# Optimization experiments

Measured on AMD Instinct MI355X. Metric: run time of the kernel, lower is better.

The kernel has to match this reference:

```python
import jax, jax.numpy as jnp
import numpy as np

LMAX = 2
C1 = 64; C2 = 64; COUT = 64
B = 4096
SUM_RDIM = sum(3**L for L in range(LMAX + 1))   # 13
FEAT1 = C1 * SUM_RDIM                            # 832
FEAT2 = C2 * SUM_RDIM


def _enumerate_paths(Lmax):
    paths = []
    for L1 in range(Lmax + 1):
        for L2 in range(Lmax + 1):
            for k in range(min(L1, L2) + 1):
                Lout = L1 + L2 - 2 * k
                if 0 <= Lout <= Lmax:
                    paths.append((L1, L2, Lout, k, False))
            if L1 >= 1 and L2 >= 1:
                for k in range(min(L1 - 1, L2 - 1) + 1):
                    Lout = L1 + L2 - 2 * k - 1
                    if 0 <= Lout <= Lmax:
                        paths.append((L1, L2, Lout, k, True))
    return paths

PATHS = _enumerate_paths(LMAX)   # 15 paths for Lmax=2


def _path_eq(L1, L2, k, use_eps):
    # Fused equation: W[c,a,b] contracted together with the delta/eps path einsum.
    letters = list('defghijklmnopqrstuvwxyz')  # a,b,c reserved for channels
    i_idx = letters[:L1]
    j_idx = letters[L1:L1 + L2]
    for r in range(k):  # delta: contract last k indices of A with last k of B
        j_idx[L2 - k + r] = i_idx[L1 - k + r]
    i_free = i_idx[:L1 - k]
    j_free = j_idx[:L2 - k]
    eps_sub = None
    if use_eps:  # consume last free index of each side via eps_{p i j}
        p = letters[L1 + L2]
        eps_sub = p + i_free[-1] + j_free[-1]
        i_free, j_free = i_free[:-1], j_free[:-1]
        out = i_free + j_free + [p]
    else:
        out = i_free + j_free
    terms = ['cab', '...a' + ''.join(i_idx), '...b' + ''.join(j_idx)]
    if eps_sub is not None:
        terms.append(eps_sub)
    return ','.join(terms) + '->...c' + ''.join(out)


def _epsilon():
    e = np.zeros((3, 3, 3), dtype=np.float32)
    e[0, 1, 2] = e[1, 2, 0] = e[2, 0, 1] = 1.0
    e[2, 1, 0] = e[1, 0, 2] = e[0, 2, 1] = -1.0
    return jnp.asarray(e)


def _split_by_rank(x, C, Lmax):
    batch = x.shape[:-1]
    out, idx = {}, 0
    for L in range(Lmax + 1):
        d = C * 3**L
        blk = x[..., idx:idx + d]
        idx += d
        out[L] = blk.reshape(*batch, C) if L == 0 else blk.reshape(*batch, C, *((3,) * L))
    return out


def setup_inputs() -> dict:
    key = jax.random.key(0)
    k1, k2, k3 = jax.random.split(key, 3)
    x1 = jax.random.normal(k1, (B, FEAT1), dtype=jnp.float32)
    x2 = jax.random.normal(k2, (B, FEAT2), dtype=jnp.float32)
    weight = jax.random.normal(k3, (len(PATHS) * COUT * C1 * C2,), dtype=jnp.float32) * 0.02
    return {"x1": x1, "x2": x2, "weight": weight}


def reference(x1, x2, weight):
    A = _split_by_rank(x1, C1, LMAX)
    Bt = _split_by_rank(x2, C2, LMAX)
    eps = _epsilon().astype(x1.dtype)
    batch = x1.shape[:-1]
    blocks = {L: jnp.zeros((*batch, COUT) + (3,) * L, dtype=x1.dtype) for L in range(LMAX + 1)}
    wsz = COUT * C1 * C2
    for n, (L1, L2, Lout, k, use_eps) in enumerate(PATHS):
        Wp = weight[n * wsz:(n + 1) * wsz].reshape(COUT, C1, C2)
        eq = _path_eq(L1, L2, k, use_eps)
        ops = (Wp, A[L1], Bt[L2]) + ((eps,) if use_eps else ())
        blocks[Lout] = blocks[Lout] + jnp.einsum(eq, *ops, optimize='optimal')
    parts = [blocks[L].reshape(*batch, COUT * 3**L) for L in range(LMAX + 1)]
    return jnp.concatenate(parts, axis=-1)
```

## Files before the change

### kernel.cpp

```cpp
#include <hip/hip_runtime.h>
#include <cstdint>
#include <cstddef>


#define FEAT 832
#define ZT 64

typedef _Float16 half8 __attribute__((ext_vector_type(8)));
typedef float floatx16 __attribute__((ext_vector_type(16)));

struct Chunk {
  int wbase;
  int o1[3];
  int o2[3];
  float sg[3];
  int d1, d2, nt;
};

__global__ void swz_w_kernel(const float* __restrict__ w, _Float16* __restrict__ o) {
  const int i = blockIdx.x * 256 + threadIdx.x;
  const int lane = i & 63;
  const int pkc  = i >> 6;
  const int cgrp = pkc & 1;
  const int ksg  = (pkc >> 1) & 255;
  const int p    = pkc >> 9;
  const int c  = cgrp * 32 + (lane & 31);
  const int k0 = ksg * 16 + (lane >> 5) * 8;
  const float* src = w + (size_t)p * 262144 + (size_t)c * 4096 + k0;
  const float4 v0 = *(const float4*)(src);
  const float4 v1 = *(const float4*)(src + 4);
  half8 h = { (_Float16)v0.x, (_Float16)v0.y, (_Float16)v0.z, (_Float16)v0.w,
              (_Float16)v1.x, (_Float16)v1.y, (_Float16)v1.z, (_Float16)v1.w };
  *(half8*)(o + (size_t)i * 8) = h;
}

__global__ __launch_bounds__(256) void gather_kernel(
    float* __restrict__ out, const float* __restrict__ part, int np)
{
  __shared__ float T[64][65];
  const int zb = blockIdx.x * 64;
  const int fb = blockIdx.y * 64;
  const int tid = threadIdx.x;
  const int fl = tid >> 6;
  const int zl = tid & 63;
  #pragma unroll
  for (int i = 0; i < 16; ++i) {
    const int f = fb + fl + i * 4;
    int s, c;
    if (f < 64)       { s = 0;              c = f; }
    else if (f < 256) { const int g = f - 64;  c = g / 3; s = 1 + g % 3; }
    else              { const int g = f - 256; c = g / 9; s = 4 + g % 9; }
    const size_t base = (size_t)s * 262144 + (size_t)c * 4096 + zb + zl;
    float v = 0.0f;
    for (int q = 0; q < np; ++q)
      v += part[(size_t)q * 3407872 + base];
    T[fl + i * 4][zl] = v;
  }
  __syncthreads();
  const int zr = tid >> 6;
  const int fc = tid & 63;
  #pragma unroll
  for (int i = 0; i < 16; ++i) {
    const int z = zr + i * 4;
    float* o = out + (size_t)(zb + z) * FEAT + fb + fc;
    *o += T[fc][z];
  }
}

__device__ __forceinline__ half8 splat8(_Float16 h) {
  return half8{h, h, h, h, h, h, h, h};
}

template<int NT>
__device__ __forceinline__ void run_chunk(
    const Chunk C, const int zbase, const int zl, const int hf,
    const int lane, const int tid, const int a0,
    const float* __restrict__ x1, const float* __restrict__ x2,
    const _Float16* __restrict__ Wh,
    _Float16* __restrict__ XS2, _Float16* __restrict__ XS1,
    floatx16& acc0, floatx16& acc1)
{
  __syncthreads();

  #pragma unroll
  for (int t = 0; t < NT; ++t) {
    const size_t base2 = (size_t)zbase * FEAT + C.o2[t];
    for (int e = tid; e < 4096; e += 256) {
      const int zz = e >> 6, b = e & 63;
      XS2[(t * 64 + zz) * 72 + b] =
          (_Float16)x2[base2 + (size_t)zz * FEAT + b * C.d2];
    }
  }
  #pragma unroll
  for (int t = 0; t < NT; ++t) {
    const float sgf = C.sg[t];
    const int o1 = C.o1[t];
    for (int e = tid; e < 4096; e += 256) {
      const int a = e & 63, zz = e >> 6;
      XS1[(t * 64 + a) * 66 + zz] =
          (_Float16)(x1[(size_t)(zbase + zz) * FEAT + o1 + a * C.d1] * sgf);
    }
  }
  __syncthreads();

  half8 x2r[NT][4];
  #pragma unroll
  for (int t = 0; t < NT; ++t) {
    #pragma unroll
    for (int ks = 0; ks < 4; ++ks)
      x2r[t][ks] = *(const half8*)&XS2[(t * 64 + zl) * 72 + ks * 16 + hf * 8];
  }

  const _Float16* __restrict__ Wq = Wh + C.wbase + lane * 8;
  const _Float16* __restrict__ Xq = XS1 + zl;

  half8 afE[2][4], afO[2][4];
  const _Float16* __restrict__ w0 = Wq + (size_t)a0 * 4096;
  #pragma unroll
  for (int ks = 0; ks < 4; ++ks) {
    afE[0][ks] = *(const half8*)(w0 + ks * 1024);
    afE[1][ks] = *(const half8*)(w0 + ks * 1024 + 512);
    afO[0][ks] = *(const half8*)(w0 + 4096 + ks * 1024);
    afO[1][ks] = *(const half8*)(w0 + 4096 + ks * 1024 + 512);
  }
  _Float16 sc[NT], scn[NT];
  #pragma unroll
  for (int t = 0; t < NT; ++t) {
    sc[t]  = Xq[(t * 64 + a0) * 66];
    scn[t] = Xq[(t * 64 + a0 + 1) * 66];
  }

  const int aend = a0 + 32;
  #pragma unroll 1
  for (int a = a0; a < aend; a += 2) {
    {
      half8 sv[NT];
      #pragma unroll
      for (int t = 0; t < NT; ++t) sv[t] = splat8(sc[t]);
      if (a + 2 < aend) {
        #pragma unroll
        for (int t = 0; t < NT; ++t) sc[t] = Xq[(t * 64 + a + 2) * 66];
      }
      #pragma unroll
      for (int ks = 0; ks < 4; ++ks) {
        half8 tb = sv[0] * x2r[0][ks];
        if (NT > 1) tb += sv[1] * x2r[1][ks];
        if (NT > 2) tb += sv[2] * x2r[2][ks];
        acc0 = __builtin_amdgcn_mfma_f32_32x32x16_f16(afE[0][ks], tb, acc0, 0, 0, 0);
        acc1 = __builtin_amdgcn_mfma_f32_32x32x16_f16(afE[1][ks], tb, acc1, 0, 0, 0);
      }
      if (a + 2 < aend) {
        const _Float16* wn = Wq + (size_t)(a + 2) * 4096;
        #pragma unroll
        for (int ks = 0; ks < 4; ++ks) {
          afE[0][ks] = *(const half8*)(wn + ks * 1024);
          afE[1][ks] = *(const half8*)(wn + ks * 1024 + 512);
        }
      }
    }
    {
      half8 sv[NT];
      #pragma unroll
      for (int t = 0; t < NT; ++t) sv[t] = splat8(scn[t]);
      if (a + 3 < aend) {
        #pragma unroll
        for (int t = 0; t < NT; ++t) scn[t] = Xq[(t * 64 + a + 3) * 66];
      }
      #pragma unroll
      for (int ks = 0; ks < 4; ++ks) {
        half8 tb = sv[0] * x2r[0][ks];
        if (NT > 1) tb += sv[1] * x2r[1][ks];
        if (NT > 2) tb += sv[2] * x2r[2][ks];
        acc0 = __builtin_amdgcn_mfma_f32_32x32x16_f16(afO[0][ks], tb, acc0, 0, 0, 0);
        acc1 = __builtin_amdgcn_mfma_f32_32x32x16_f16(afO[1][ks], tb, acc1, 0, 0, 0);
      }
      if (a + 3 < aend) {
        const _Float16* wn = Wq + (size_t)(a + 3) * 4096;
        #pragma unroll
        for (int ks = 0; ks < 4; ++ks) {
          afO[0][ks] = *(const half8*)(wn + ks * 1024);
          afO[1][ks] = *(const half8*)(wn + ks * 1024 + 512);
        }
      }
    }
  }
}

__global__ __launch_bounds__(256, 2) void tp_kernel(
    const float* __restrict__ x1, const float* __restrict__ x2,
    const _Float16* __restrict__ Wh, float* __restrict__ out,
    float* __restrict__ part)
{
  __shared__ __align__(16) _Float16 XS2[3 * 64 * 72];
  __shared__ __align__(16) _Float16 XS1[3 * 64 * 66];
  __shared__ Chunk chs[7];
  __shared__ int nch_s;

  const int tid  = threadIdx.x;
  const int slot = blockIdx.y;
  const int q    = blockIdx.z;
  const int nsplit = gridDim.z;
  const int zbase = blockIdx.x * ZT;
  const int wid  = tid >> 6;
  const int zgrp = wid & 1;
  const int ah   = wid >> 1;
  const int a0   = ah * 32;
  const int lane = tid & 63;
  const int ln31 = lane & 31;
  const int hf   = lane >> 5;
  const int zl   = zgrp * 32 + ln31;

  int offO, dO, mO;
  if (slot == 0)      { offO = 0;   dO = 1; mO = 0; }
  else if (slot < 4)  { offO = 64;  dO = 3; mO = slot - 1; }
  else                { offO = 256; dO = 9; mO = slot - 4; }

  if (tid == 0) {
    int n = 0;
    auto add = [&](int p, int L1, int L2,
                   int i0, int i1, int i2, int j0, int j1, int j2,
                   float s0, float s1, float s2, int nt) {
      const int offs[3] = {0, 64, 256};
      const int ds[3]   = {1, 3, 9};
      Chunk c;
      c.wbase = p * 262144;
      c.o1[0] = offs[L1] + i0; c.o1[1] = offs[L1] + i1; c.o1[2] = offs[L1] + i2;
      c.o2[0] = offs[L2] + j0; c.o2[1] = offs[L2] + j1; c.o2[2] = offs[L2] + j2;
      c.sg[0] = s0; c.sg[1] = s1; c.sg[2] = s2;
      c.d1 = ds[L1]; c.d2 = ds[L2]; c.nt = nt;
      chs[n++] = c;
    };
    if (slot == 0) {
      add(0, 0,0, 0,0,0, 0,0,0, 1,0,0, 1);
      add(5, 1,1, 0,1,2, 0,1,2, 1,1,1, 3);
      add(13,2,2, 0,1,2, 0,1,2, 1,1,1, 3);
      add(13,2,2, 3,4,5, 3,4,5, 1,1,1, 3);
      add(13,2,2, 6,7,8, 6,7,8, 1,1,1, 3);
    } else if (slot < 4) {
      const int m = slot - 1, p1 = (m+1)%3, p2 = (m+2)%3;
      add(1, 0,1, 0,0,0, m,0,0, 1,0,0, 1);
      add(3, 1,0, m,0,0, 0,0,0, 1,0,0, 1);
      add(6, 1,1, p1,p2,0, p2,p1,0, 1,-1,0, 2);
      add(7, 1,2, 0,1,2, 3*m,3*m+1,3*m+2, 1,1,1, 3);
      add(10,2,1, 3*m,3*m+1,3*m+2, 0,1,2, 1,1,1, 3);
      add(14,2,2, 3*p1,3*p1+1,3*p1+2, 3*p2,3*p2+1,3*p2+2, 1,1,1, 3);
      add(14,2,2, 3*p2,3*p2+1,3*p2+2, 3*p1,3*p1+1,3*p1+2, -1,-1,-1, 3);
    } else {
      const int m = slot - 4, u = m/3, v = m%3, q1 = (v+1)%3, q2 = (v+2)%3;
      add(2, 0,2, 0,0,0, m,0,0, 1,0,0, 1);
      add(4, 1,1, u,0,0, v,0,0, 1,0,0, 1);
      add(8, 1,2, q1,q2,0, 3*u+q2,3*u+q1,0, 1,-1,0, 2);
      add(9, 2,0, m,0,0, 0,0,0, 1,0,0, 1);
      add(11,2,1, 3*u+q1,3*u+q2,0, q2,q1,0, 1,-1,0, 2);
      add(12,2,2, 3*u,3*u+1,3*u+2, 3*v,3*v+1,3*v+2, 1,1,1, 3);
    }
    nch_s = n;
  }
  __syncthreads();
  const int nch = nch_s;

  floatx16 acc0, acc1;
  #pragma unroll
  for (int r = 0; r < 16; ++r) { acc0[r] = 0.0f; acc1[r] = 0.0f; }

  for (int ci = q; ci < nch; ci += nsplit) {
    const Chunk C = chs[ci];
    if (C.nt == 1)      run_chunk<1>(C, zbase, zl, hf, lane, tid, a0, x1, x2, Wh, XS2, XS1, acc0, acc1);
    else if (C.nt == 2) run_chunk<2>(C, zbase, zl, hf, lane, tid, a0, x1, x2, Wh, XS2, XS1, acc0, acc1);
    else                run_chunk<3>(C, zbase, zl, hf, lane, tid, a0, x1, x2, Wh, XS2, XS1, acc0, acc1);
  }

  __syncthreads();
  float* R = (float*)XS2;
  if (ah == 1) {
    #pragma unroll
    for (int r = 0; r < 16; ++r) {
      R[r * 128 + zgrp * 64 + lane]        = acc0[r];
      R[(16 + r) * 128 + zgrp * 64 + lane] = acc1[r];
    }
  }
  __syncthreads();
  if (ah == 0) {
    #pragma unroll
    for (int r = 0; r < 16; ++r) {
      acc0[r] += R[r * 128 + zgrp * 64 + lane];
      acc1[r] += R[(16 + r) * 128 + zgrp * 64 + lane];
    }

    if (q == 0) {
      float* __restrict__ op = out + (size_t)(zbase + zl) * FEAT + offO + mO;
      #pragma unroll
      for (int r = 0; r < 16; ++r) {
        const int cr = (r & 3) + 8 * (r >> 2) + 4 * hf;
        op[(size_t)cr * dO]        = acc0[r];
        op[(size_t)(cr + 32) * dO] = acc1[r];
      }
    } else {
      float* __restrict__ op = part + (size_t)(q - 1) * 3407872
                                    + (size_t)slot * 262144 + (zbase + zl);
      #pragma unroll
      for (int r = 0; r < 16; ++r) {
        const int cr = (r & 3) + 8 * (r >> 2) + 4 * hf;
        op[(size_t)cr * 4096]        = acc0[r];
        op[(size_t)(cr + 32) * 4096] = acc1[r];
      }
    }
  }
}

extern "C" void kernel_launch(void* const* d_in, const int* in_sizes, int n_in,
                              void* d_out, int out_size, void* d_ws, size_t ws_size,
                              hipStream_t stream) {
  const float* x1 = (const float*)d_in[0];
  const float* x2 = (const float*)d_in[1];
  const float* w  = (const float*)d_in[2];
  float* out = (float*)d_out;
  _Float16* Wh = (_Float16*)d_ws;
  float* part = (float*)((char*)d_ws + 7864320);

  const size_t plane_bytes = 3407872ull * 4ull;
  int np = (ws_size > 7864320) ? (int)((ws_size - 7864320) / plane_bytes) : 1;
  if (np > 3) np = 3;
  if (np < 1) np = 1;
  const int nsplit = np + 1;

  const int nchunks = 15 * 64 * 4096 / 8;
  hipLaunchKernelGGL(swz_w_kernel, dim3(nchunks / 256), dim3(256), 0, stream, w, Wh);

  dim3 grid(64, 13, nsplit);
  hipLaunchKernelGGL(tp_kernel, grid, dim3(256), 0, stream, x1, x2, Wh, out, part);

  dim3 ggrid(64, 13);
  hipLaunchKernelGGL(gather_kernel, ggrid, dim3(256), 0, stream, out, part, np);
}
```

Measured before the change: 420.0 us.

## Merge z-groups into one wave to reuse weight fragments across both z halves

Shrinks the tp_kernel block from four waves to two. Each wave now covers both 32-row z halves with four accumulators instead of two, so every weight fragment loaded from global memory feeds two MFMAs instead of one, halving per-block weight traffic. The cost is higher register pressure (four 16-float accumulators plus doubled x2 fragments), fewer threads for the shared-memory staging loops, and fewer waves per block for latency hiding.

Result: faster. 411.3 us (-2.1%).

```diff
diff --git a/kernel.cpp b/kernel.cpp
--- a/kernel.cpp
+++ b/kernel.cpp
@@ -73,19 +73,19 @@
 
 template<int NT>
 __device__ __forceinline__ void run_chunk(
-    const Chunk C, const int zbase, const int zl, const int hf,
+    const Chunk C, const int zbase, const int ln31, const int hf,
     const int lane, const int tid, const int a0,
     const float* __restrict__ x1, const float* __restrict__ x2,
     const _Float16* __restrict__ Wh,
     _Float16* __restrict__ XS2, _Float16* __restrict__ XS1,
-    floatx16& acc0, floatx16& acc1)
+    floatx16& acc00, floatx16& acc01, floatx16& acc10, floatx16& acc11)
 {
   __syncthreads();
 
   #pragma unroll
   for (int t = 0; t < NT; ++t) {
     const size_t base2 = (size_t)zbase * FEAT + C.o2[t];
-    for (int e = tid; e < 4096; e += 256) {
+    for (int e = tid; e < 4096; e += 128) {
       const int zz = e >> 6, b = e & 63;
       XS2[(t * 64 + zz) * 72 + b] =
           (_Float16)x2[base2 + (size_t)zz * FEAT + b * C.d2];
@@ -95,7 +95,7 @@
   for (int t = 0; t < NT; ++t) {
     const float sgf = C.sg[t];
     const int o1 = C.o1[t];
-    for (int e = tid; e < 4096; e += 256) {
+    for (int e = tid; e < 4096; e += 128) {
       const int a = e & 63, zz = e >> 6;
       XS1[(t * 64 + a) * 66 + zz] =
           (_Float16)(x1[(size_t)(zbase + zz) * FEAT + o1 + a * C.d1] * sgf);
@@ -103,16 +103,18 @@
   }
   __syncthreads();
 
-  half8 x2r[NT][4];
-  #pragma unroll
-  for (int t = 0; t < NT; ++t) {
+  half8 x2r[NT][2][4];
+  #pragma unroll
+  for (int t = 0; t < NT; ++t)
     #pragma unroll
-    for (int ks = 0; ks < 4; ++ks)
-      x2r[t][ks] = *(const half8*)&XS2[(t * 64 + zl) * 72 + ks * 16 + hf * 8];
-  }
+    for (int zh = 0; zh < 2; ++zh)
+      #pragma unroll
+      for (int ks = 0; ks < 4; ++ks)
+        x2r[t][zh][ks] =
+            *(const half8*)&XS2[(t * 64 + zh * 32 + ln31) * 72 + ks * 16 + hf * 8];
 
   const _Float16* __restrict__ Wq = Wh + C.wbase + lane * 8;
-  const _Float16* __restrict__ Xq = XS1 + zl;
+  const _Float16* __restrict__ Xq = XS1 + ln31;
 
   half8 afE[2][4], afO[2][4];
   const _Float16* __restrict__ w0 = Wq + (size_t)a0 * 4096;
@@ -123,31 +125,42 @@
     afO[0][ks] = *(const half8*)(w0 + 4096 + ks * 1024);
     afO[1][ks] = *(const half8*)(w0 + 4096 + ks * 1024 + 512);
   }
-  _Float16 sc[NT], scn[NT];
-  #pragma unroll
-  for (int t = 0; t < NT; ++t) {
-    sc[t]  = Xq[(t * 64 + a0) * 66];
-    scn[t] = Xq[(t * 64 + a0 + 1) * 66];
-  }
+  _Float16 sc[NT][2], scn[NT][2];
+  #pragma unroll
+  for (int t = 0; t < NT; ++t)
+    #pragma unroll
+    for (int zh = 0; zh < 2; ++zh) {
+      sc[t][zh]  = Xq[(t * 64 + a0) * 66 + zh * 32];
+      scn[t][zh] = Xq[(t * 64 + a0 + 1) * 66 + zh * 32];
+    }
 
   const int aend = a0 + 32;
   #pragma unroll 1
   for (int a = a0; a < aend; a += 2) {
     {
-      half8 sv[NT];
-      #pragma unroll
-      for (int t = 0; t < NT; ++t) sv[t] = splat8(sc[t]);
+      half8 sv[NT][2];
+      #pragma unroll
+      for (int t = 0; t < NT; ++t) {
+        sv[t][0] = splat8(sc[t][0]);
+        sv[t][1] = splat8(sc[t][1]);
+      }
       if (a + 2 < aend) {
         #pragma unroll
-        for (int t = 0; t < NT; ++t) sc[t] = Xq[(t * 64 + a + 2) * 66];
+        for (int t = 0; t < NT; ++t) {
+          sc[t][0] = Xq[(t * 64 + a + 2) * 66];
+          sc[t][1] = Xq[(t * 64 + a + 2) * 66 + 32];
+        }
       }
       #pragma unroll
       for (int ks = 0; ks < 4; ++ks) {
-        half8 tb = sv[0] * x2r[0][ks];
-        if (NT > 1) tb += sv[1] * x2r[1][ks];
-        if (NT > 2) tb += sv[2] * x2r[2][ks];
-        acc0 = __builtin_amdgcn_mfma_f32_32x32x16_f16(afE[0][ks], tb, acc0, 0, 0, 0);
-        acc1 = __builtin_amdgcn_mfma_f32_32x32x16_f16(afE[1][ks], tb, acc1, 0, 0, 0);
+        half8 tb0 = sv[0][0] * x2r[0][0][ks];
+        half8 tb1 = sv[0][1] * x2r[0][1][ks];
+        if (NT > 1) { tb0 += sv[1][0] * x2r[1][0][ks]; tb1 += sv[1][1] * x2r[1][1][ks]; }
+        if (NT > 2) { tb0 += sv[2][0] * x2r[2][0][ks]; tb1 += sv[2][1] * x2r[2][1][ks]; }
+        acc00 = __builtin_amdgcn_mfma_f32_32x32x16_f16(afE[0][ks], tb0, acc00, 0, 0, 0);
+        acc01 = __builtin_amdgcn_mfma_f32_32x32x16_f16(afE[0][ks], tb1, acc01, 0, 0, 0);
+        acc10 = __builtin_amdgcn_mfma_f32_32x32x16_f16(afE[1][ks], tb0, acc10, 0, 0, 0);
+        acc11 = __builtin_amdgcn_mfma_f32_32x32x16_f16(afE[1][ks], tb1, acc11, 0, 0, 0);
       }
       if (a + 2 < aend) {
         const _Float16* wn = Wq + (size_t)(a + 2) * 4096;
@@ -159,20 +172,29 @@
       }
     }
     {
-      half8 sv[NT];
-      #pragma unroll
-      for (int t = 0; t < NT; ++t) sv[t] = splat8(scn[t]);
+      half8 sv[NT][2];
+      #pragma unroll
+      for (int t = 0; t < NT; ++t) {
+        sv[t][0] = splat8(scn[t][0]);
+        sv[t][1] = splat8(scn[t][1]);
+      }
       if (a + 3 < aend) {
         #pragma unroll
-        for (int t = 0; t < NT; ++t) scn[t] = Xq[(t * 64 + a + 3) * 66];
+        for (int t = 0; t < NT; ++t) {
+          scn[t][0] = Xq[(t * 64 + a + 3) * 66];
+          scn[t][1] = Xq[(t * 64 + a + 3) * 66 + 32];
+        }
       }
       #pragma unroll
       for (int ks = 0; ks < 4; ++ks) {
-        half8 tb = sv[0] * x2r[0][ks];
-        if (NT > 1) tb += sv[1] * x2r[1][ks];
-        if (NT > 2) tb += sv[2] * x2r[2][ks];
-        acc0 = __builtin_amdgcn_mfma_f32_32x32x16_f16(afO[0][ks], tb, acc0, 0, 0, 0);
-        acc1 = __builtin_amdgcn_mfma_f32_32x32x16_f16(afO[1][ks], tb, acc1, 0, 0, 0);
+        half8 tb0 = sv[0][0] * x2r[0][0][ks];
+        half8 tb1 = sv[0][1] * x2r[0][1][ks];
+        if (NT > 1) { tb0 += sv[1][0] * x2r[1][0][ks]; tb1 += sv[1][1] * x2r[1][1][ks]; }
+        if (NT > 2) { tb0 += sv[2][0] * x2r[2][0][ks]; tb1 += sv[2][1] * x2r[2][1][ks]; }
+        acc00 = __builtin_amdgcn_mfma_f32_32x32x16_f16(afO[0][ks], tb0, acc00, 0, 0, 0);
+        acc01 = __builtin_amdgcn_mfma_f32_32x32x16_f16(afO[0][ks], tb1, acc01, 0, 0, 0);
+        acc10 = __builtin_amdgcn_mfma_f32_32x32x16_f16(afO[1][ks], tb0, acc10, 0, 0, 0);
+        acc11 = __builtin_amdgcn_mfma_f32_32x32x16_f16(afO[1][ks], tb1, acc11, 0, 0, 0);
       }
       if (a + 3 < aend) {
         const _Float16* wn = Wq + (size_t)(a + 3) * 4096;
@@ -186,7 +208,7 @@
   }
 }
 
-__global__ __launch_bounds__(256, 2) void tp_kernel(
+__global__ __launch_bounds__(128, 2) void tp_kernel(
     const float* __restrict__ x1, const float* __restrict__ x2,
     const _Float16* __restrict__ Wh, float* __restrict__ out,
     float* __restrict__ part)
@@ -201,14 +223,11 @@
   const int q    = blockIdx.z;
   const int nsplit = gridDim.z;
   const int zbase = blockIdx.x * ZT;
-  const int wid  = tid >> 6;
-  const int zgrp = wid & 1;
-  const int ah   = wid >> 1;
+  const int ah   = tid >> 6;
   const int a0   = ah * 32;
   const int lane = tid & 63;
   const int ln31 = lane & 31;
   const int hf   = lane >> 5;
-  const int zl   = zgrp * 32 + ln31;
 
   int offO, dO, mO;
   if (slot == 0)      { offO = 0;   dO = 1; mO = 0; }
@@ -259,15 +278,23 @@
   __syncthreads();
   const int nch = nch_s;
 
-  floatx16 acc0, acc1;
-  #pragma unroll
-  for (int r = 0; r < 16; ++r) { acc0[r] = 0.0f; acc1[r] = 0.0f; }
+  floatx16 acc00, acc01, acc10, acc11;
+  #pragma unroll
+  for (int r = 0; r < 16; ++r) {
+    acc00[r] = 0.0f; acc01[r] = 0.0f; acc10[r] = 0.0f; acc11[r] = 0.0f;
+  }
 
   for (int ci = q; ci < nch; ci += nsplit) {
     const Chunk C = chs[ci];
-    if (C.nt == 1)      run_chunk<1>(C, zbase, zl, hf, lane, tid, a0, x1, x2, Wh, XS2, XS1, acc0, acc1);
-    else if (C.nt == 2) run_chunk<2>(C, zbase, zl, hf, lane, tid, a0, x1, x2, Wh, XS2, XS1, acc0, acc1);
-    else                run_chunk<3>(C, zbase, zl, hf, lane, tid, a0, x1, x2, Wh, XS2, XS1, acc0, acc1);
+    if (C.nt == 1)
+      run_chunk<1>(C, zbase, ln31, hf, lane, tid, a0, x1, x2, Wh, XS2, XS1,
+                   acc00, acc01, acc10, acc11);
+    else if (C.nt == 2)
+      run_chunk<2>(C, zbase, ln31, hf, lane, tid, a0, x1, x2, Wh, XS2, XS1,
+                   acc00, acc01, acc10, acc11);
+    else
+      run_chunk<3>(C, zbase, ln31, hf, lane, tid, a0, x1, x2, Wh, XS2, XS1,
+                   acc00, acc01, acc10, acc11);
   }
 
   __syncthreads();
@@ -275,34 +302,44 @@
   if (ah == 1) {
     #pragma unroll
     for (int r = 0; r < 16; ++r) {
-      R[r * 128 + zgrp * 64 + lane]        = acc0[r];
-      R[(16 + r) * 128 + zgrp * 64 + lane] = acc1[r];
+      R[(0 * 16 + r) * 64 + lane] = acc00[r];
+      R[(1 * 16 + r) * 64 + lane] = acc01[r];
+      R[(2 * 16 + r) * 64 + lane] = acc10[r];
+      R[(3 * 16 + r) * 64 + lane] = acc11[r];
     }
   }
   __syncthreads();
   if (ah == 0) {
     #pragma unroll
     for (int r = 0; r < 16; ++r) {
-      acc0[r] += R[r * 128 + zgrp * 64 + lane];
-      acc1[r] += R[(16 + r) * 128 + zgrp * 64 + lane];
+      acc00[r] += R[(0 * 16 + r) * 64 + lane];
+      acc01[r] += R[(1 * 16 + r) * 64 + lane];
+      acc10[r] += R[(2 * 16 + r) * 64 + lane];
+      acc11[r] += R[(3 * 16 + r) * 64 + lane];
     }
 
     if (q == 0) {
-      float* __restrict__ op = out + (size_t)(zbase + zl) * FEAT + offO + mO;
+      float* __restrict__ op0 = out + (size_t)(zbase + ln31) * FEAT + offO + mO;
+      float* __restrict__ op1 = out + (size_t)(zbase + 32 + ln31) * FEAT + offO + mO;
       #pragma unroll
       for (int r = 0; r < 16; ++r) {
         const int cr = (r & 3) + 8 * (r >> 2) + 4 * hf;
-        op[(size_t)cr * dO]        = acc0[r];
-        op[(size_t)(cr + 32) * dO] = acc1[r];
+        op0[(size_t)cr * dO]        = acc00[r];
+        op0[(size_t)(cr + 32) * dO] = acc10[r];
+        op1[(size_t)cr * dO]        = acc01[r];
+        op1[(size_t)(cr + 32) * dO] = acc11[r];
       }
     } else {
-      float* __restrict__ op = part + (size_t)(q - 1) * 3407872
-                                    + (size_t)slot * 262144 + (zbase + zl);
+      float* __restrict__ op0 = part + (size_t)(q - 1) * 3407872
+                                     + (size_t)slot * 262144 + (zbase + ln31);
+      float* __restrict__ op1 = op0 + 32;
       #pragma unroll
       for (int r = 0; r < 16; ++r) {
         const int cr = (r & 3) + 8 * (r >> 2) + 4 * hf;
-        op[(size_t)cr * 4096]        = acc0[r];
-        op[(size_t)(cr + 32) * 4096] = acc1[r];
+        op0[(size_t)cr * 4096]        = acc00[r];
+        op0[(size_t)(cr + 32) * 4096] = acc10[r];
+        op1[(size_t)cr * 4096]        = acc01[r];
+        op1[(size_t)(cr + 32) * 4096] = acc11[r];
       }
     }
   }
@@ -328,7 +365,7 @@
   hipLaunchKernelGGL(swz_w_kernel, dim3(nchunks / 256), dim3(256), 0, stream, w, Wh);
 
   dim3 grid(64, 13, nsplit);
-  hipLaunchKernelGGL(tp_kernel, grid, dim3(256), 0, stream, x1, x2, Wh, out, part);
+  hipLaunchKernelGGL(tp_kernel, grid, dim3(128), 0, stream, x1, x2, Wh, out, part);
 
   dim3 ggrid(64, 13);
   hipLaunchKernelGGL(gather_kernel, ggrid, dim3(256), 0, stream, out, part, np);
```

## Drop split-K over chunks and gather pass; add MFMA priority hints

Applied to the files above, without the earlier changes.

Removes the split of each output slot's chunk list across grid.z blocks, along with the partial-sum workspace and the separate gather/reduction kernel. Each block now processes all chunks for its slot and writes the output directly. The change also wraps the MFMA loops in s_setprio raising and lowering. This removes the partial-plane writes and re-reads and one kernel launch, but cuts the grid from 832 times nsplit blocks to 832 blocks, which lowers parallelism and lengthens each block's serial work.

After: 373.5 us. -11.1%, faster.

```diff
diff --git a/kernel.cpp b/kernel.cpp
--- a/kernel.cpp
+++ b/kernel.cpp
@@ -34,39 +34,6 @@
   *(half8*)(o + (size_t)i * 8) = h;
 }
 
-__global__ __launch_bounds__(256) void gather_kernel(
-    float* __restrict__ out, const float* __restrict__ part, int np)
-{
-  __shared__ float T[64][65];
-  const int zb = blockIdx.x * 64;
-  const int fb = blockIdx.y * 64;
-  const int tid = threadIdx.x;
-  const int fl = tid >> 6;
-  const int zl = tid & 63;
-  #pragma unroll
-  for (int i = 0; i < 16; ++i) {
-    const int f = fb + fl + i * 4;
-    int s, c;
-    if (f < 64)       { s = 0;              c = f; }
-    else if (f < 256) { const int g = f - 64;  c = g / 3; s = 1 + g % 3; }
-    else              { const int g = f - 256; c = g / 9; s = 4 + g % 9; }
-    const size_t base = (size_t)s * 262144 + (size_t)c * 4096 + zb + zl;
-    float v = 0.0f;
-    for (int q = 0; q < np; ++q)
-      v += part[(size_t)q * 3407872 + base];
-    T[fl + i * 4][zl] = v;
-  }
-  __syncthreads();
-  const int zr = tid >> 6;
-  const int fc = tid & 63;
-  #pragma unroll
-  for (int i = 0; i < 16; ++i) {
-    const int z = zr + i * 4;
-    float* o = out + (size_t)(zb + z) * FEAT + fb + fc;
-    *o += T[fc][z];
-  }
-}
-
 __device__ __forceinline__ half8 splat8(_Float16 h) {
   return half8{h, h, h, h, h, h, h, h};
 }
@@ -141,14 +108,17 @@
         #pragma unroll
         for (int t = 0; t < NT; ++t) sc[t] = Xq[(t * 64 + a + 2) * 66];
       }
+      half8 tb = sv[0] * x2r[0][0];
+      __builtin_amdgcn_s_setprio(1);
       #pragma unroll
       for (int ks = 0; ks < 4; ++ks) {
-        half8 tb = sv[0] * x2r[0][ks];
+        tb = sv[0] * x2r[0][ks];
         if (NT > 1) tb += sv[1] * x2r[1][ks];
         if (NT > 2) tb += sv[2] * x2r[2][ks];
         acc0 = __builtin_amdgcn_mfma_f32_32x32x16_f16(afE[0][ks], tb, acc0, 0, 0, 0);
         acc1 = __builtin_amdgcn_mfma_f32_32x32x16_f16(afE[1][ks], tb, acc1, 0, 0, 0);
       }
+      __builtin_amdgcn_s_setprio(0);
       if (a + 2 < aend) {
         const _Float16* wn = Wq + (size_t)(a + 2) * 4096;
         #pragma unroll
@@ -166,6 +136,7 @@
         #pragma unroll
         for (int t = 0; t < NT; ++t) scn[t] = Xq[(t * 64 + a + 3) * 66];
       }
+      __builtin_amdgcn_s_setprio(1);
       #pragma unroll
       for (int ks = 0; ks < 4; ++ks) {
         half8 tb = sv[0] * x2r[0][ks];
@@ -174,6 +145,7 @@
         acc0 = __builtin_amdgcn_mfma_f32_32x32x16_f16(afO[0][ks], tb, acc0, 0, 0, 0);
         acc1 = __builtin_amdgcn_mfma_f32_32x32x16_f16(afO[1][ks], tb, acc1, 0, 0, 0);
       }
+      __builtin_amdgcn_s_setprio(0);
       if (a + 3 < aend) {
         const _Float16* wn = Wq + (size_t)(a + 3) * 4096;
         #pragma unroll
@@ -188,8 +160,7 @@
 
 __global__ __launch_bounds__(256, 2) void tp_kernel(
     const float* __restrict__ x1, const float* __restrict__ x2,
-    const _Float16* __restrict__ Wh, float* __restrict__ out,
-    float* __restrict__ part)
+    const _Float16* __restrict__ Wh, float* __restrict__ out)
 {
   __shared__ __align__(16) _Float16 XS2[3 * 64 * 72];
   __shared__ __align__(16) _Float16 XS1[3 * 64 * 66];
@@ -198,8 +169,6 @@
 
   const int tid  = threadIdx.x;
   const int slot = blockIdx.y;
-  const int q    = blockIdx.z;
-  const int nsplit = gridDim.z;
   const int zbase = blockIdx.x * ZT;
   const int wid  = tid >> 6;
   const int zgrp = wid & 1;
@@ -263,7 +232,7 @@
   #pragma unroll
   for (int r = 0; r < 16; ++r) { acc0[r] = 0.0f; acc1[r] = 0.0f; }
 
-  for (int ci = q; ci < nch; ci += nsplit) {
+  for (int ci = 0; ci < nch; ++ci) {
     const Chunk C = chs[ci];
     if (C.nt == 1)      run_chunk<1>(C, zbase, zl, hf, lane, tid, a0, x1, x2, Wh, XS2, XS1, acc0, acc1);
     else if (C.nt == 2) run_chunk<2>(C, zbase, zl, hf, lane, tid, a0, x1, x2, Wh, XS2, XS1, acc0, acc1);
@@ -287,23 +256,12 @@
       acc1[r] += R[(16 + r) * 128 + zgrp * 64 + lane];
     }
 
-    if (q == 0) {
-      float* __restrict__ op = out + (size_t)(zbase + zl) * FEAT + offO + mO;
-      #pragma unroll
-      for (int r = 0; r < 16; ++r) {
-        const int cr = (r & 3) + 8 * (r >> 2) + 4 * hf;
-        op[(size_t)cr * dO]        = acc0[r];
-        op[(size_t)(cr + 32) * dO] = acc1[r];
-      }
-    } else {
-      float* __restrict__ op = part + (size_t)(q - 1) * 3407872
-                                    + (size_t)slot * 262144 + (zbase + zl);
-      #pragma unroll
-      for (int r = 0; r < 16; ++r) {
-        const int cr = (r & 3) + 8 * (r >> 2) + 4 * hf;
-        op[(size_t)cr * 4096]        = acc0[r];
-        op[(size_t)(cr + 32) * 4096] = acc1[r];
-      }
+    float* __restrict__ op = out + (size_t)(zbase + zl) * FEAT + offO + mO;
+    #pragma unroll
+    for (int r = 0; r < 16; ++r) {
+      const int cr = (r & 3) + 8 * (r >> 2) + 4 * hf;
+      op[(size_t)cr * dO]        = acc0[r];
+      op[(size_t)(cr + 32) * dO] = acc1[r];
     }
   }
 }
@@ -316,20 +274,10 @@
   const float* w  = (const float*)d_in[2];
   float* out = (float*)d_out;
   _Float16* Wh = (_Float16*)d_ws;
-  float* part = (float*)((char*)d_ws + 7864320);
-
-  const size_t plane_bytes = 3407872ull * 4ull;
-  int np = (ws_size > 7864320) ? (int)((ws_size - 7864320) / plane_bytes) : 1;
-  if (np > 3) np = 3;
-  if (np < 1) np = 1;
-  const int nsplit = np + 1;
 
   const int nchunks = 15 * 64 * 4096 / 8;
   hipLaunchKernelGGL(swz_w_kernel, dim3(nchunks / 256), dim3(256), 0, stream, w, Wh);
 
-  dim3 grid(64, 13, nsplit);
-  hipLaunchKernelGGL(tp_kernel, grid, dim3(256), 0, stream, x1, x2, Wh, out, part);
-
-  dim3 ggrid(64, 13);
-  hipLaunchKernelGGL(gather_kernel, ggrid, dim3(256), 0, stream, out, part, np);
-}
+  dim3 grid(64, 13);
+  hipLaunchKernelGGL(tp_kernel, grid, dim3(256), 0, stream, x1, x2, Wh, out);
+}
```
